# Optimization experiments

Hardware: AMD Instinct MI355X
Metric: run time of the kernel (lower is better)

Reference implementation:

```python
import jax, jax.numpy as jnp
import numpy as np
from math import sqrt

D_LLM = 768
N_HEADS = 8
D_KEYS = 128


def setup_inputs() -> dict:
    key = jax.random.key(0)
    ks = jax.random.split(key, 9)
    B, T, N, S = 8, 96, 16, 1000
    dkh = D_KEYS * N_HEADS
    inp = {
        "time_series": jax.random.normal(ks[0], (B, T, N), dtype=jnp.float32),
        "source_embedding": jax.random.normal(ks[1], (S, D_LLM), dtype=jnp.float32),
        "value_embedding": jax.random.normal(ks[2], (S, D_LLM), dtype=jnp.float32),
        # key_projection: Linear(d_llm, d_keys*n_heads)
        "Wk": jax.random.normal(ks[3], (D_LLM, dkh), dtype=jnp.float32) / np.float32(sqrt(D_LLM)),
        "bk": jnp.zeros((dkh,), dtype=jnp.float32),
        # value_projection: Linear(d_llm, d_keys*n_heads)
        "Wv": jax.random.normal(ks[4], (D_LLM, dkh), dtype=jnp.float32) / np.float32(sqrt(D_LLM)),
        "bv": jnp.zeros((dkh,), dtype=jnp.float32),
        # out_projection: Linear(d_keys*n_heads, d_llm)
        "Wo": jax.random.normal(ks[5], (dkh, D_LLM), dtype=jnp.float32) / np.float32(sqrt(dkh)),
        "bo": jnp.zeros((D_LLM,), dtype=jnp.float32),
    }
    return inp


def reference(time_series, source_embedding, value_embedding, Wk, bk, Wv, bv, Wo, bo):
    B, T, N = time_series.shape
    S = source_embedding.shape[0]
    H, dk = N_HEADS, D_KEYS

    # (B,T,N) -> (B*N, T); Q repeats each scalar across d_keys*n_heads then nan->0
    ts = jnp.transpose(time_series, (0, 2, 1)).reshape(B * N, T)
    ts = jnp.where(jnp.isnan(ts), jnp.float32(0.0), ts)
    Q = jnp.broadcast_to(ts[:, :, None, None], (B * N, T, H, dk))  # bthe

    K = (source_embedding @ Wk + bk).reshape(S, H, dk)  # she
    V = (value_embedding @ Wv + bv).reshape(S, H, dk)   # she

    scale = jnp.float32(1.0 / sqrt(dk))
    scores = jnp.einsum('bthe,she->bhts', Q, K)          # [B*N, H, T, S]
    A = jax.nn.softmax(scale * scores, axis=-1)          # dropout = identity (eval)
    out = jnp.einsum('bhts,she->bthe', A, V).reshape(B * N, T, H * dk)
    return out @ Wo + bo                                 # [B*N, T, d_llm]
```

## Files before the change

kernel.cpp:

```cpp
#include <hip/hip_runtime.h>
#include <hip/hip_bf16.h>
#include <math.h>

#define D_LLM 768
#define DKH   1024
#define NH    8
#define DK    128
#define S_LEN 1000
#define S_PAD 1024
#define M_ROWS 12288
#define T_LEN 96
#define N_VARS 16

static constexpr float SCALE_EXP2 = (float)(0.08838834764831845 * 1.4426950408889634);

typedef __attribute__((ext_vector_type(8))) _Float16 half8;
typedef __attribute__((ext_vector_type(2))) _Float16 half2v;
typedef __attribute__((ext_vector_type(4))) float f32x4;

__device__ __forceinline__ half2v pkrtz(float a, float b) {
    return __builtin_bit_cast(half2v, __builtin_amdgcn_cvt_pkrtz(a, b));
}

__device__ __forceinline__ void gload_lds16(const void* g, void* l) {
    __builtin_amdgcn_global_load_lds(
        (const __attribute__((address_space(1))) unsigned int*)g,
        (__attribute__((address_space(3))) unsigned int*)l, 16, 0, 0);
}

__global__ __launch_bounds__(256) void prep_kernel(const float* __restrict__ vemb,
                                                   const float* __restrict__ Wv,
                                                   const float* __restrict__ Wo,
                                                   const float* __restrict__ Wk,
                                                   const float* __restrict__ bk,
                                                   _Float16* __restrict__ Ab16,
                                                   _Float16* __restrict__ Wvt,
                                                   _Float16* __restrict__ Wot,
                                                   float* __restrict__ Wksum,
                                                   float* __restrict__ bksum) {
    __shared__ float tl[32][33];
    int blk = blockIdx.x, tid = threadIdx.x;
    if (blk < 768) {
        int i4 = (blk * 256 + tid) * 4;
        float4 v = make_float4(0.f, 0.f, 0.f, 0.f);
        if (i4 < S_LEN * D_LLM) v = *(const float4*)(vemb + i4);
        short4 o;
        o.x = __builtin_bit_cast(short, (_Float16)v.x);
        o.y = __builtin_bit_cast(short, (_Float16)v.y);
        o.z = __builtin_bit_cast(short, (_Float16)v.z);
        o.w = __builtin_bit_cast(short, (_Float16)v.w);
        *(short4*)(Ab16 + i4) = o;
    } else if (blk < 1536) {
        int tau = blk - 768;
        int k0 = (tau % 24) * 32, n0 = (tau / 24) * 32;
        int tx = tid & 31, ty = tid >> 5;
        #pragma unroll
        for (int p = 0; p < 4; ++p)
            tl[ty + p * 8][tx] = Wv[(size_t)(k0 + ty + p * 8) * DKH + n0 + tx];
        __syncthreads();
        #pragma unroll
        for (int p = 0; p < 4; ++p)
            Wvt[(size_t)(n0 + ty + p * 8) * D_LLM + k0 + tx] = (_Float16)tl[tx][ty + p * 8];
    } else if (blk < 2304) {
        int tau = blk - 1536;
        int k0 = (tau & 31) * 32, n0 = (tau >> 5) * 32;
        int tx = tid & 31, ty = tid >> 5;
        #pragma unroll
        for (int p = 0; p < 4; ++p)
            tl[ty + p * 8][tx] = Wo[(size_t)(k0 + ty + p * 8) * D_LLM + n0 + tx];
        __syncthreads();
        #pragma unroll
        for (int p = 0; p < 4; ++p)
            Wot[(size_t)(n0 + ty + p * 8) * DKH + k0 + tx] = (_Float16)tl[tx][ty + p * 8];
    } else {
        int blk2 = blk - 2304;
        int w = tid >> 6, lane = tid & 63;
        if (blk2 < 192) {
            int d = blk2 * 4 + w;
            const float* p = Wk + (size_t)d * DKH + lane * 16;
            float s = 0.f;
            #pragma unroll
            for (int i = 0; i < 4; ++i) {
                float4 v = *(const float4*)(p + i * 4);
                s += v.x + v.y + v.z + v.w;
            }
            s += __shfl_down(s, 4);
            s += __shfl_down(s, 2);
            s += __shfl_down(s, 1);
            if ((lane & 7) == 0) Wksum[d * NH + (lane >> 3)] = s;
        } else if (w == 0) {
            const float* p = bk + lane * 16;
            float s = 0.f;
            #pragma unroll
            for (int i = 0; i < 4; ++i) {
                float4 v = *(const float4*)(p + i * 4);
                s += v.x + v.y + v.z + v.w;
            }
            s += __shfl_down(s, 4);
            s += __shfl_down(s, 2);
            s += __shfl_down(s, 1);
            if ((lane & 7) == 0) bksum[lane >> 3] = s;
        }
    }
}

__global__ __launch_bounds__(256) void ksum_kernel(const float* __restrict__ src,
                                                   const float* __restrict__ Wksum,
                                                   const float* __restrict__ bksum,
                                                   float* __restrict__ Kpad) {
    int w = threadIdx.x >> 6, lane = threadIdx.x & 63;
    int s = blockIdx.x * 4 + w;
    if (s >= S_LEN) {
        if (lane < 8) Kpad[lane * S_PAD + s] = 0.f;
        return;
    }
    const float* sp = src + (size_t)s * D_LLM + lane * 12;
    float xv[12];
    ((float4*)xv)[0] = *(const float4*)(sp);
    ((float4*)xv)[1] = *(const float4*)(sp + 4);
    ((float4*)xv)[2] = *(const float4*)(sp + 8);
    float a[8] = {0.f, 0.f, 0.f, 0.f, 0.f, 0.f, 0.f, 0.f};
    const float* wp = Wksum + lane * 12 * NH;
    #pragma unroll
    for (int i = 0; i < 12; ++i) {
        float4 wa = *(const float4*)(wp + i * 8);
        float4 wb = *(const float4*)(wp + i * 8 + 4);
        a[0] = fmaf(xv[i], wa.x, a[0]); a[1] = fmaf(xv[i], wa.y, a[1]);
        a[2] = fmaf(xv[i], wa.z, a[2]); a[3] = fmaf(xv[i], wa.w, a[3]);
        a[4] = fmaf(xv[i], wb.x, a[4]); a[5] = fmaf(xv[i], wb.y, a[5]);
        a[6] = fmaf(xv[i], wb.z, a[6]); a[7] = fmaf(xv[i], wb.w, a[7]);
    }
    #pragma unroll
    for (int off = 32; off > 0; off >>= 1) {
        #pragma unroll
        for (int hh = 0; hh < 8; ++hh) a[hh] += __shfl_xor(a[hh], off);
    }
    #pragma unroll
    for (int hh = 0; hh < 8; ++hh)
        if (lane == hh) Kpad[hh * S_PAD + s] = (a[hh] + bksum[hh]) * SCALE_EXP2;
}

__global__ __launch_bounds__(64) void kminmax_kernel(const float* __restrict__ Kpad,
                                                     float* __restrict__ mnmx) {
    int h = blockIdx.x, lane = threadIdx.x;
    float mx = -1e30f, mn = 1e30f;
    for (int s = lane; s < S_LEN; s += 64) {
        float v = Kpad[h * S_PAD + s];
        mx = fmaxf(mx, v); mn = fminf(mn, v);
    }
    #pragma unroll
    for (int off = 32; off > 0; off >>= 1) {
        mx = fmaxf(mx, __shfl_xor(mx, off));
        mn = fminf(mn, __shfl_xor(mn, off));
    }
    if (lane == 0) { mnmx[h * 2] = mn; mnmx[h * 2 + 1] = mx; }
}

__global__ __launch_bounds__(256) void vproj_kernel(const _Float16* __restrict__ A,
                                                    const _Float16* __restrict__ Bt,
                                                    const float* __restrict__ bias,
                                                    _Float16* __restrict__ Vt) {
    __shared__ _Float16 As[2][64 * 32];
    __shared__ _Float16 Bs[2][64 * 32];
    int t = threadIdx.x, w = t >> 6, lane = t & 63;
    int bm0 = (blockIdx.x >> 4) * 64, bn0 = (blockIdx.x & 15) * 64;
    int lrow = t >> 2, lcol = (t & 3) * 8;
    const _Float16* ga = A + (size_t)(bm0 + lrow) * D_LLM + lcol;
    const _Float16* gb = Bt + (size_t)(bn0 + lrow) * D_LLM + lcol;

    f32x4 acc[2][2];
    #pragma unroll
    for (int m = 0; m < 2; ++m)
        #pragma unroll
        for (int n = 0; n < 2; ++n) acc[m][n] = (f32x4){0.f, 0.f, 0.f, 0.f};
    int sgrp = (lane >> 4) << 3;
    int arow = (w >> 1) * 32 + (lane & 15);
    int brow = (w & 1) * 32 + (lane & 15);

#define VSTAGE(buf, k0) do { \
        gload_lds16(ga + (k0), (char*)&As[buf][0] + w * 1024); \
        gload_lds16(gb + (k0), (char*)&Bs[buf][0] + w * 1024); } while (0)

    VSTAGE(0, 0);
    __syncthreads();
    #pragma unroll 2
    for (int tt = 0; tt < 24; ++tt) {
        int cur = tt & 1;
        if (tt < 23) VSTAGE(cur ^ 1, (tt + 1) * 32);
        const _Float16* Ac = &As[cur][0];
        const _Float16* Bc = &Bs[cur][0];
        half8 af[2], bf[2];
        #pragma unroll
        for (int m = 0; m < 2; ++m) af[m] = *(const half8*)(Ac + (arow + m * 16) * 32 + sgrp);
        #pragma unroll
        for (int n = 0; n < 2; ++n) bf[n] = *(const half8*)(Bc + (brow + n * 16) * 32 + sgrp);
        __builtin_amdgcn_s_setprio(1);
        #pragma unroll
        for (int m = 0; m < 2; ++m)
            #pragma unroll
            for (int n = 0; n < 2; ++n)
                acc[m][n] = __builtin_amdgcn_mfma_f32_16x16x32_f16(af[m], bf[n], acc[m][n], 0, 0, 0);
        __builtin_amdgcn_s_setprio(0);
        __syncthreads();
    }
#undef VSTAGE

    int rowoff = (lane >> 4) << 2;
    #pragma unroll
    for (int m = 0; m < 2; ++m) {
        #pragma unroll
        for (int n = 0; n < 2; ++n) {
            int c = bn0 + (w & 1) * 32 + n * 16 + (lane & 15);
            float b = bias[c];
            #pragma unroll
            for (int q = 0; q < 4; ++q) {
                int srow = bm0 + (w >> 1) * 32 + m * 16 + rowoff + q;
                float val = (srow < S_LEN) ? acc[m][n][q] + b : 0.f;
                Vt[(size_t)c * S_PAD + srow] = (_Float16)val;
            }
        }
    }
}

__device__ __forceinline__ void compute_afr(const float* kq, float x0, float x1,
                                            float nm0, float nm1, half8& o0, half8& o1) {
    float4 a = *(const float4*)kq;
    float4 b = *(const float4*)(kq + 4);
    float kv[8] = {a.x, a.y, a.z, a.w, b.x, b.y, b.z, b.w};
    union { half8 v; half2v h[4]; } u0, u1;
    #pragma unroll
    for (int j = 0; j < 4; ++j) {
        float w00 = __builtin_amdgcn_exp2f(fmaf(x0, kv[2 * j], nm0));
        float w01 = __builtin_amdgcn_exp2f(fmaf(x0, kv[2 * j + 1], nm0));
        u0.h[j] = pkrtz(w00, w01);
        float w10 = __builtin_amdgcn_exp2f(fmaf(x1, kv[2 * j], nm1));
        float w11 = __builtin_amdgcn_exp2f(fmaf(x1, kv[2 * j + 1], nm1));
        u1.h[j] = pkrtz(w10, w11);
    }
    o0 = u0.v; o1 = u1.v;
}

__global__ __launch_bounds__(256) void attn_mfma_kernel(const float* __restrict__ ts,
                                                        const float* __restrict__ Kpad,
                                                        const float* __restrict__ mnmx,
                                                        const _Float16* __restrict__ Vt,
                                                        _Float16* __restrict__ attB) {
    __shared__ _Float16 Vs[2][8192];
    const int tid = threadIdx.x;
    const int lane = tid & 63, w = tid >> 6;
    const int h = blockIdx.y;
    const int m0 = (blockIdx.x * 4 + w) * 32;
    const int l15 = lane & 15, q = lane >> 4;

    const int erow = w * 8 + (lane >> 3);
    const int sgl = ((lane & 7) ^ (lane >> 3)) * 8;
    const _Float16* gsrc = Vt + (size_t)(h * DK + erow) * S_PAD + sgl;

    float mn = mnmx[h * 2], mx = mnmx[h * 2 + 1];
    float x0, x1, nm0, nm1;
    {
        int m = m0 + l15;
        int rr = m / T_LEN;
        float v = ts[((size_t)(rr >> 4) * T_LEN + (m % T_LEN)) * N_VARS + (rr & 15)];
        x0 = (v != v) ? 0.f : v;
        nm0 = -((x0 >= 0.f) ? x0 * mx : x0 * mn);
        m = m0 + 16 + l15;
        rr = m / T_LEN;
        v = ts[((size_t)(rr >> 4) * T_LEN + (m % T_LEN)) * N_VARS + (rr & 15)];
        x1 = (v != v) ? 0.f : v;
        nm1 = -((x1 >= 0.f) ? x1 * mx : x1 * mn);
    }
    float wpadf0, wpadf1;
    {
        half2v p0 = pkrtz(__builtin_amdgcn_exp2f(nm0), 0.f);
        half2v p1 = pkrtz(__builtin_amdgcn_exp2f(nm1), 0.f);
        wpadf0 = (float)p0[0];
        wpadf1 = (float)p1[0];
    }

    f32x4 acc0[8], acc1[8];
    #pragma unroll
    for (int e = 0; e < 8; ++e) {
        acc0[e] = (f32x4){0.f, 0.f, 0.f, 0.f};
        acc1[e] = (f32x4){0.f, 0.f, 0.f, 0.f};
    }
    f32x4 accd0 = (f32x4){0.f, 0.f, 0.f, 0.f};
    f32x4 accd1 = (f32x4){0.f, 0.f, 0.f, 0.f};
    half8 ones;
    #pragma unroll
    for (int j = 0; j < 8; ++j) ones[j] = (_Float16)1.0f;

    const float* kvp = Kpad + h * S_PAD + q * 8;
    half8 afrA0, afrA1, afrB0, afrB1;
    compute_afr(kvp, x0, x1, nm0, nm1, afrA0, afrA1);

    #pragma unroll
    for (int i = 0; i < 4; ++i)
        gload_lds16(gsrc + (size_t)(i * 32) * S_PAD, (char*)&Vs[0][0] + i * 4096 + w * 1024);
    #pragma unroll
    for (int i = 0; i < 4; ++i)
        gload_lds16(gsrc + (size_t)(i * 32) * S_PAD + 64, (char*)&Vs[1][0] + i * 4096 + w * 1024);
    asm volatile("s_waitcnt vmcnt(4)" ::: "memory");
    __builtin_amdgcn_s_barrier();

    const int bofs0 = l15 * 128 + ((q * 16) ^ ((l15 & 7) << 4));
    const int bofs1 = l15 * 128 + ((64 + q * 16) ^ ((l15 & 7) << 4));

#define PVSTEP(AF0, AF1, BOFS) do { \
        __builtin_amdgcn_s_setprio(1); \
        _Pragma("unroll") \
        for (int e = 0; e < 8; ++e) { \
            half8 bfv = *(const half8*)(cb + e * 2048 + (BOFS)); \
            acc0[e] = __builtin_amdgcn_mfma_f32_16x16x32_f16(AF0, bfv, acc0[e], 0, 0, 0); \
            acc1[e] = __builtin_amdgcn_mfma_f32_16x16x32_f16(AF1, bfv, acc1[e], 0, 0, 0); \
        } \
        accd0 = __builtin_amdgcn_mfma_f32_16x16x32_f16(AF0, ones, accd0, 0, 0, 0); \
        accd1 = __builtin_amdgcn_mfma_f32_16x16x32_f16(AF1, ones, accd1, 0, 0, 0); \
        __builtin_amdgcn_s_setprio(0); } while (0)

    #pragma unroll 2
    for (int kt = 0; kt < 16; ++kt) {
        const char* cb = (const char*)&Vs[0][0] + (kt & 1) * 16384;
        compute_afr(kvp + kt * 64 + 32, x0, x1, nm0, nm1, afrB0, afrB1);
        PVSTEP(afrA0, afrA1, bofs0);
        if (kt < 15) compute_afr(kvp + (kt + 1) * 64, x0, x1, nm0, nm1, afrA0, afrA1);
        PVSTEP(afrB0, afrB1, bofs1);
        __builtin_amdgcn_s_barrier();
        if (kt < 14) {
            #pragma unroll
            for (int i = 0; i < 4; ++i)
                gload_lds16(gsrc + (size_t)(i * 32) * S_PAD + (kt + 2) * 64,
                            (char*)&Vs[0][0] + (kt & 1) * 16384 + i * 4096 + w * 1024);
            asm volatile("s_waitcnt vmcnt(4)" ::: "memory");
        } else {
            asm volatile("s_waitcnt vmcnt(0)" ::: "memory");
        }
        __builtin_amdgcn_s_barrier();
    }
#undef PVSTEP

    int rowoff = q << 2;
    #pragma unroll
    for (int r = 0; r < 2; ++r) {
        #pragma unroll
        for (int qq = 0; qq < 4; ++qq) {
            float wp = __shfl(r ? wpadf1 : wpadf0, rowoff + qq);
            float den = (r ? accd1[qq] : accd0[qq]) - 24.f * wp;
            float inv = 1.f / den;
            int mrow = m0 + r * 16 + rowoff + qq;
            _Float16* op = attB + (size_t)mrow * DKH + h * DK + l15;
            #pragma unroll
            for (int e = 0; e < 8; ++e)
                op[e * 16] = (_Float16)((r ? acc1[e][qq] : acc0[e][qq]) * inv);
        }
    }
}

__global__ __launch_bounds__(256) void outproj_kernel(const _Float16* __restrict__ A,
                                                      const _Float16* __restrict__ Bt,
                                                      const float* __restrict__ bo,
                                                      float* __restrict__ C) {
    __shared__ _Float16 As[2][128 * 32];
    __shared__ _Float16 Bs[2][96 * 32];
    int wg = blockIdx.x;
    wg = (wg & 7) * 96 + (wg >> 3);
    int bx = wg & 7, by = wg >> 3;
    int t = threadIdx.x, w = t >> 6, lane = t & 63;
    int bm0 = by * 128, bn0 = bx * 96;
    int lrow = t >> 2, lcol = (t & 3) * 8;
    const _Float16* ga0 = A + (size_t)(bm0 + lrow) * DKH + lcol;
    const _Float16* ga1 = ga0 + (size_t)64 * DKH;
    const _Float16* gb0 = Bt + (size_t)(bn0 + lrow) * DKH + lcol;
    const _Float16* gb1 = gb0 + (size_t)64 * DKH;

    f32x4 acc[4][3];
    #pragma unroll
    for (int m = 0; m < 4; ++m)
        #pragma unroll
        for (int n = 0; n < 3; ++n) acc[m][n] = (f32x4){0.f, 0.f, 0.f, 0.f};

    int sgrp = (lane >> 4) << 3;
    int arow = (w >> 1) * 64 + (lane & 15);
    int brow = (w & 1) * 48 + (lane & 15);

#define OSTAGE(buf, k0) do { \
        gload_lds16(ga0 + (k0), (char*)&As[buf][0] + w * 1024); \
        gload_lds16(ga1 + (k0), (char*)&As[buf][0] + 4096 + w * 1024); \
        gload_lds16(gb0 + (k0), (char*)&Bs[buf][0] + w * 1024); \
        if (w < 2) gload_lds16(gb1 + (k0), (char*)&Bs[buf][0] + 4096 + w * 1024); } while (0)

    OSTAGE(0, 0);
    __syncthreads();
    #pragma unroll 2
    for (int tt = 0; tt < 32; ++tt) {
        int cur = tt & 1;
        if (tt < 31) OSTAGE(cur ^ 1, (tt + 1) * 32);
        const _Float16* Ac = &As[cur][0];
        const _Float16* Bc = &Bs[cur][0];
        half8 af[4], bf[3];
        #pragma unroll
        for (int m = 0; m < 4; ++m) af[m] = *(const half8*)(Ac + (arow + m * 16) * 32 + sgrp);
        #pragma unroll
        for (int n = 0; n < 3; ++n) bf[n] = *(const half8*)(Bc + (brow + n * 16) * 32 + sgrp);
        __builtin_amdgcn_s_setprio(1);
        #pragma unroll
        for (int m = 0; m < 4; ++m)
            #pragma unroll
            for (int n = 0; n < 3; ++n)
                acc[m][n] = __builtin_amdgcn_mfma_f32_16x16x32_f16(af[m], bf[n], acc[m][n], 0, 0, 0);
        __builtin_amdgcn_s_setprio(0);
        __syncthreads();
    }
#undef OSTAGE

    int rowoff = (lane >> 4) << 2;
    #pragma unroll
    for (int m = 0; m < 4; ++m) {
        #pragma unroll
        for (int n = 0; n < 3; ++n) {
            int col = bn0 + (w & 1) * 48 + n * 16 + (lane & 15);
            float b = bo[col];
            #pragma unroll
            for (int q = 0; q < 4; ++q) {
                int row = bm0 + (w >> 1) * 64 + m * 16 + rowoff + q;
                C[(size_t)row * D_LLM + col] = acc[m][n][q] + b;
            }
        }
    }
}

extern "C" void kernel_launch(void* const* d_in, const int* in_sizes, int n_in,
                              void* d_out, int out_size, void* d_ws, size_t ws_size,
                              hipStream_t stream) {
    const float* ts   = (const float*)d_in[0];
    const float* src  = (const float*)d_in[1];
    const float* vemb = (const float*)d_in[2];
    const float* Wk   = (const float*)d_in[3];
    const float* bk   = (const float*)d_in[4];
    const float* Wv   = (const float*)d_in[5];
    const float* bv   = (const float*)d_in[6];
    const float* Wo   = (const float*)d_in[7];
    const float* bo   = (const float*)d_in[8];
    float* out = (float*)d_out;

    float* ws = (float*)d_ws;
    float* Kpad   = ws;
    float* Wksum  = ws + 8192;
    float* bksum  = ws + 14336;
    float* mnmx   = ws + 14352;
    _Float16* Vt   = (_Float16*)(ws + 14592);
    _Float16* Wot  = (_Float16*)(ws + 540672);
    _Float16* attB = (_Float16*)(ws + 936960);
    _Float16* Ab16 = (_Float16*)(ws + 936960);
    _Float16* Wvt  = (_Float16*)(ws + 1330176);

    prep_kernel<<<2497, 256, 0, stream>>>(vemb, Wv, Wo, Wk, bk, Ab16, Wvt, Wot, Wksum, bksum);
    ksum_kernel<<<256, 256, 0, stream>>>(src, Wksum, bksum, Kpad);
    kminmax_kernel<<<8, 64, 0, stream>>>(Kpad, mnmx);
    vproj_kernel<<<256, 256, 0, stream>>>(Ab16, Wvt, bv, Vt);
    {
        dim3 g(96, NH);
        attn_mfma_kernel<<<g, 256, 0, stream>>>(ts, Kpad, mnmx, Vt, attB);
    }
    outproj_kernel<<<768, 256, 0, stream>>>(attB, Wot, bo, out);
}
```

Baseline: 100.8 us.

## Merge K-sum and V-projection kernels, fold min/max into attention, triple-buffer loads

Merges the K row-sum kernel and the V projection GEMM into one launch split by block index, and drops the separate min/max kernel. Each attention block now loads its K row into LDS and computes the per-head min/max itself. The attention and output-projection loops move from double to triple-buffered LDS staging with one barrier per iteration and explicit vmcnt waits, so global loads overlap compute more. This removes two launches and some barriers, at the cost of more LDS per block (possible occupancy loss) and redundant min/max work in every attention block.

```diff
diff --git a/kernel.cpp b/kernel.cpp
--- a/kernel.cpp
+++ b/kernel.cpp
@@ -104,67 +104,54 @@
     }
 }
 
-__global__ __launch_bounds__(256) void ksum_kernel(const float* __restrict__ src,
-                                                   const float* __restrict__ Wksum,
-                                                   const float* __restrict__ bksum,
-                                                   float* __restrict__ Kpad) {
-    int w = threadIdx.x >> 6, lane = threadIdx.x & 63;
-    int s = blockIdx.x * 4 + w;
-    if (s >= S_LEN) {
-        if (lane < 8) Kpad[lane * S_PAD + s] = 0.f;
+__global__ __launch_bounds__(256) void kv_kernel(const float* __restrict__ src,
+                                                 const float* __restrict__ Wksum,
+                                                 const float* __restrict__ bksum,
+                                                 float* __restrict__ Kpad,
+                                                 const _Float16* __restrict__ A,
+                                                 const _Float16* __restrict__ Bt,
+                                                 const float* __restrict__ bias,
+                                                 _Float16* __restrict__ Vt) {
+    __shared__ _Float16 VAs[2][2048];
+    __shared__ _Float16 VBs[2][2048];
+    int tid = threadIdx.x;
+    if (blockIdx.x < 256) {
+        int w = tid >> 6, lane = tid & 63;
+        int s = blockIdx.x * 4 + w;
+        if (s >= S_LEN) {
+            if (lane < 8) Kpad[lane * S_PAD + s] = 0.f;
+            return;
+        }
+        const float* sp = src + (size_t)s * D_LLM + lane * 12;
+        float xv[12];
+        ((float4*)xv)[0] = *(const float4*)(sp);
+        ((float4*)xv)[1] = *(const float4*)(sp + 4);
+        ((float4*)xv)[2] = *(const float4*)(sp + 8);
+        float a[8] = {0.f, 0.f, 0.f, 0.f, 0.f, 0.f, 0.f, 0.f};
+        const float* wp = Wksum + lane * 12 * NH;
+        #pragma unroll
+        for (int i = 0; i < 12; ++i) {
+            float4 wa = *(const float4*)(wp + i * 8);
+            float4 wb = *(const float4*)(wp + i * 8 + 4);
+            a[0] = fmaf(xv[i], wa.x, a[0]); a[1] = fmaf(xv[i], wa.y, a[1]);
+            a[2] = fmaf(xv[i], wa.z, a[2]); a[3] = fmaf(xv[i], wa.w, a[3]);
+            a[4] = fmaf(xv[i], wb.x, a[4]); a[5] = fmaf(xv[i], wb.y, a[5]);
+            a[6] = fmaf(xv[i], wb.z, a[6]); a[7] = fmaf(xv[i], wb.w, a[7]);
+        }
+        #pragma unroll
+        for (int off = 32; off > 0; off >>= 1) {
+            #pragma unroll
+            for (int hh = 0; hh < 8; ++hh) a[hh] += __shfl_xor(a[hh], off);
+        }
+        #pragma unroll
+        for (int hh = 0; hh < 8; ++hh)
+            if (lane == hh) Kpad[hh * S_PAD + s] = (a[hh] + bksum[hh]) * SCALE_EXP2;
         return;
     }
-    const float* sp = src + (size_t)s * D_LLM + lane * 12;
-    float xv[12];
-    ((float4*)xv)[0] = *(const float4*)(sp);
-    ((float4*)xv)[1] = *(const float4*)(sp + 4);
-    ((float4*)xv)[2] = *(const float4*)(sp + 8);
-    float a[8] = {0.f, 0.f, 0.f, 0.f, 0.f, 0.f, 0.f, 0.f};
-    const float* wp = Wksum + lane * 12 * NH;
-    #pragma unroll
-    for (int i = 0; i < 12; ++i) {
-        float4 wa = *(const float4*)(wp + i * 8);
-        float4 wb = *(const float4*)(wp + i * 8 + 4);
-        a[0] = fmaf(xv[i], wa.x, a[0]); a[1] = fmaf(xv[i], wa.y, a[1]);
-        a[2] = fmaf(xv[i], wa.z, a[2]); a[3] = fmaf(xv[i], wa.w, a[3]);
-        a[4] = fmaf(xv[i], wb.x, a[4]); a[5] = fmaf(xv[i], wb.y, a[5]);
-        a[6] = fmaf(xv[i], wb.z, a[6]); a[7] = fmaf(xv[i], wb.w, a[7]);
-    }
-    #pragma unroll
-    for (int off = 32; off > 0; off >>= 1) {
-        #pragma unroll
-        for (int hh = 0; hh < 8; ++hh) a[hh] += __shfl_xor(a[hh], off);
-    }
-    #pragma unroll
-    for (int hh = 0; hh < 8; ++hh)
-        if (lane == hh) Kpad[hh * S_PAD + s] = (a[hh] + bksum[hh]) * SCALE_EXP2;
-}
-
-__global__ __launch_bounds__(64) void kminmax_kernel(const float* __restrict__ Kpad,
-                                                     float* __restrict__ mnmx) {
-    int h = blockIdx.x, lane = threadIdx.x;
-    float mx = -1e30f, mn = 1e30f;
-    for (int s = lane; s < S_LEN; s += 64) {
-        float v = Kpad[h * S_PAD + s];
-        mx = fmaxf(mx, v); mn = fminf(mn, v);
-    }
-    #pragma unroll
-    for (int off = 32; off > 0; off >>= 1) {
-        mx = fmaxf(mx, __shfl_xor(mx, off));
-        mn = fminf(mn, __shfl_xor(mn, off));
-    }
-    if (lane == 0) { mnmx[h * 2] = mn; mnmx[h * 2 + 1] = mx; }
-}
-
-__global__ __launch_bounds__(256) void vproj_kernel(const _Float16* __restrict__ A,
-                                                    const _Float16* __restrict__ Bt,
-                                                    const float* __restrict__ bias,
-                                                    _Float16* __restrict__ Vt) {
-    __shared__ _Float16 As[2][64 * 32];
-    __shared__ _Float16 Bs[2][64 * 32];
-    int t = threadIdx.x, w = t >> 6, lane = t & 63;
-    int bm0 = (blockIdx.x >> 4) * 64, bn0 = (blockIdx.x & 15) * 64;
-    int lrow = t >> 2, lcol = (t & 3) * 8;
+    int b2 = blockIdx.x - 256;
+    int w = tid >> 6, lane = tid & 63;
+    int bm0 = (b2 >> 4) * 64, bn0 = (b2 & 15) * 64;
+    int lrow = tid >> 2, lcol = (tid & 3) * 8;
     const _Float16* ga = A + (size_t)(bm0 + lrow) * D_LLM + lcol;
     const _Float16* gb = Bt + (size_t)(bn0 + lrow) * D_LLM + lcol;
 
@@ -178,8 +165,8 @@
     int brow = (w & 1) * 32 + (lane & 15);
 
 #define VSTAGE(buf, k0) do { \
-        gload_lds16(ga + (k0), (char*)&As[buf][0] + w * 1024); \
-        gload_lds16(gb + (k0), (char*)&Bs[buf][0] + w * 1024); } while (0)
+        gload_lds16(ga + (k0), (char*)&VAs[buf][0] + w * 1024); \
+        gload_lds16(gb + (k0), (char*)&VBs[buf][0] + w * 1024); } while (0)
 
     VSTAGE(0, 0);
     __syncthreads();
@@ -187,8 +174,8 @@
     for (int tt = 0; tt < 24; ++tt) {
         int cur = tt & 1;
         if (tt < 23) VSTAGE(cur ^ 1, (tt + 1) * 32);
-        const _Float16* Ac = &As[cur][0];
-        const _Float16* Bc = &Bs[cur][0];
+        const _Float16* Ac = &VAs[cur][0];
+        const _Float16* Bc = &VBs[cur][0];
         half8 af[2], bf[2];
         #pragma unroll
         for (int m = 0; m < 2; ++m) af[m] = *(const half8*)(Ac + (arow + m * 16) * 32 + sgrp);
@@ -242,10 +229,11 @@
 
 __global__ __launch_bounds__(256) void attn_mfma_kernel(const float* __restrict__ ts,
                                                         const float* __restrict__ Kpad,
-                                                        const float* __restrict__ mnmx,
                                                         const _Float16* __restrict__ Vt,
                                                         _Float16* __restrict__ attB) {
-    __shared__ _Float16 Vs[2][8192];
+    __shared__ _Float16 Vs[3][8192];
+    __shared__ float Krow[1024];
+    __shared__ float red[8];
     const int tid = threadIdx.x;
     const int lane = tid & 63, w = tid >> 6;
     const int h = blockIdx.y;
@@ -255,21 +243,54 @@
     const int erow = w * 8 + (lane >> 3);
     const int sgl = ((lane & 7) ^ (lane >> 3)) * 8;
     const _Float16* gsrc = Vt + (size_t)(h * DK + erow) * S_PAD + sgl;
-
-    float mn = mnmx[h * 2], mx = mnmx[h * 2 + 1];
-    float x0, x1, nm0, nm1;
+    const float* kg = Kpad + h * S_PAD;
+
+    gload_lds16(kg + w * 256 + lane * 4, (char*)Krow + w * 1024);
+    #pragma unroll
+    for (int i = 0; i < 4; ++i)
+        gload_lds16(gsrc + (size_t)(i * 32) * S_PAD, (char*)&Vs[0][0] + i * 4096 + w * 1024);
+    #pragma unroll
+    for (int i = 0; i < 4; ++i)
+        gload_lds16(gsrc + (size_t)(i * 32) * S_PAD + 64, (char*)&Vs[1][0] + i * 4096 + w * 1024);
+
+    float x0, x1;
     {
         int m = m0 + l15;
         int rr = m / T_LEN;
         float v = ts[((size_t)(rr >> 4) * T_LEN + (m % T_LEN)) * N_VARS + (rr & 15)];
         x0 = (v != v) ? 0.f : v;
-        nm0 = -((x0 >= 0.f) ? x0 * mx : x0 * mn);
         m = m0 + 16 + l15;
         rr = m / T_LEN;
         v = ts[((size_t)(rr >> 4) * T_LEN + (m % T_LEN)) * N_VARS + (rr & 15)];
         x1 = (v != v) ? 0.f : v;
-        nm1 = -((x1 >= 0.f) ? x1 * mx : x1 * mn);
-    }
+    }
+
+    asm volatile("s_waitcnt vmcnt(8)" ::: "memory");
+    __builtin_amdgcn_sched_barrier(0);
+    __builtin_amdgcn_s_barrier();
+
+    float mn, mx;
+    {
+        float4 k4 = *(const float4*)&Krow[tid * 4];
+        if (tid < 250) {
+            mx = fmaxf(fmaxf(k4.x, k4.y), fmaxf(k4.z, k4.w));
+            mn = fminf(fminf(k4.x, k4.y), fminf(k4.z, k4.w));
+        } else { mx = -3e38f; mn = 3e38f; }
+        #pragma unroll
+        for (int off = 32; off > 0; off >>= 1) {
+            mx = fmaxf(mx, __shfl_xor(mx, off));
+            mn = fminf(mn, __shfl_xor(mn, off));
+        }
+        if (lane == 0) { red[w * 2] = mn; red[w * 2 + 1] = mx; }
+        asm volatile("s_waitcnt lgkmcnt(0)" ::: "memory");
+        __builtin_amdgcn_sched_barrier(0);
+        __builtin_amdgcn_s_barrier();
+        mn = fminf(fminf(red[0], red[2]), fminf(red[4], red[6]));
+        mx = fmaxf(fmaxf(red[1], red[3]), fmaxf(red[5], red[7]));
+    }
+
+    float nm0 = -((x0 >= 0.f) ? x0 * mx : x0 * mn);
+    float nm1 = -((x1 >= 0.f) ? x1 * mx : x1 * mn);
     float wpadf0, wpadf1;
     {
         half2v p0 = pkrtz(__builtin_amdgcn_exp2f(nm0), 0.f);
@@ -290,18 +311,9 @@
     #pragma unroll
     for (int j = 0; j < 8; ++j) ones[j] = (_Float16)1.0f;
 
-    const float* kvp = Kpad + h * S_PAD + q * 8;
+    const float* kvp = Krow + q * 8;
     half8 afrA0, afrA1, afrB0, afrB1;
     compute_afr(kvp, x0, x1, nm0, nm1, afrA0, afrA1);
-
-    #pragma unroll
-    for (int i = 0; i < 4; ++i)
-        gload_lds16(gsrc + (size_t)(i * 32) * S_PAD, (char*)&Vs[0][0] + i * 4096 + w * 1024);
-    #pragma unroll
-    for (int i = 0; i < 4; ++i)
-        gload_lds16(gsrc + (size_t)(i * 32) * S_PAD + 64, (char*)&Vs[1][0] + i * 4096 + w * 1024);
-    asm volatile("s_waitcnt vmcnt(4)" ::: "memory");
-    __builtin_amdgcn_s_barrier();
 
     const int bofs0 = l15 * 128 + ((q * 16) ^ ((l15 & 7) << 4));
     const int bofs1 = l15 * 128 + ((64 + q * 16) ^ ((l15 & 7) << 4));
@@ -318,24 +330,23 @@
         accd1 = __builtin_amdgcn_mfma_f32_16x16x32_f16(AF1, ones, accd1, 0, 0, 0); \
         __builtin_amdgcn_s_setprio(0); } while (0)
 
-    #pragma unroll 2
+    #pragma unroll
     for (int kt = 0; kt < 16; ++kt) {
-        const char* cb = (const char*)&Vs[0][0] + (kt & 1) * 16384;
+        if (kt == 15) asm volatile("s_waitcnt vmcnt(0)" ::: "memory");
+        else         asm volatile("s_waitcnt vmcnt(4)" ::: "memory");
+        __builtin_amdgcn_sched_barrier(0);
+        __builtin_amdgcn_s_barrier();
+        if (kt < 14) {
+            char* d = (char*)&Vs[0][0] + ((kt + 2) % 3) * 16384 + w * 1024;
+            #pragma unroll
+            for (int i = 0; i < 4; ++i)
+                gload_lds16(gsrc + (size_t)(i * 32) * S_PAD + (kt + 2) * 64, d + i * 4096);
+        }
+        const char* cb = (const char*)&Vs[0][0] + (kt % 3) * 16384;
         compute_afr(kvp + kt * 64 + 32, x0, x1, nm0, nm1, afrB0, afrB1);
         PVSTEP(afrA0, afrA1, bofs0);
         if (kt < 15) compute_afr(kvp + (kt + 1) * 64, x0, x1, nm0, nm1, afrA0, afrA1);
         PVSTEP(afrB0, afrB1, bofs1);
-        __builtin_amdgcn_s_barrier();
-        if (kt < 14) {
-            #pragma unroll
-            for (int i = 0; i < 4; ++i)
-                gload_lds16(gsrc + (size_t)(i * 32) * S_PAD + (kt + 2) * 64,
-                            (char*)&Vs[0][0] + (kt & 1) * 16384 + i * 4096 + w * 1024);
-            asm volatile("s_waitcnt vmcnt(4)" ::: "memory");
-        } else {
-            asm volatile("s_waitcnt vmcnt(0)" ::: "memory");
-        }
-        __builtin_amdgcn_s_barrier();
     }
 #undef PVSTEP
 
@@ -360,8 +371,8 @@
                                                       const _Float16* __restrict__ Bt,
                                                       const float* __restrict__ bo,
                                                       float* __restrict__ C) {
-    __shared__ _Float16 As[2][128 * 32];
-    __shared__ _Float16 Bs[2][96 * 32];
+    __shared__ _Float16 As[3][4096];
+    __shared__ _Float16 Bs[3][3072];
     int wg = blockIdx.x;
     wg = (wg & 7) * 96 + (wg >> 3);
     int bx = wg & 7, by = wg >> 3;
@@ -383,20 +394,24 @@
     int arow = (w >> 1) * 64 + (lane & 15);
     int brow = (w & 1) * 48 + (lane & 15);
 
-#define OSTAGE(buf, k0) do { \
-        gload_lds16(ga0 + (k0), (char*)&As[buf][0] + w * 1024); \
-        gload_lds16(ga1 + (k0), (char*)&As[buf][0] + 4096 + w * 1024); \
-        gload_lds16(gb0 + (k0), (char*)&Bs[buf][0] + w * 1024); \
-        if (w < 2) gload_lds16(gb1 + (k0), (char*)&Bs[buf][0] + 4096 + w * 1024); } while (0)
+#define OSTAGE(bi, k0) do { \
+        gload_lds16(ga0 + (k0), (char*)&As[bi][0] + w * 1024); \
+        gload_lds16(ga1 + (k0), (char*)&As[bi][0] + 4096 + w * 1024); \
+        gload_lds16(gb0 + (k0), (char*)&Bs[bi][0] + w * 1024); \
+        if (w < 2) gload_lds16(gb1 + (k0), (char*)&Bs[bi][0] + 4096 + w * 1024); } while (0)
 
     OSTAGE(0, 0);
-    __syncthreads();
-    #pragma unroll 2
-    for (int tt = 0; tt < 32; ++tt) {
-        int cur = tt & 1;
-        if (tt < 31) OSTAGE(cur ^ 1, (tt + 1) * 32);
-        const _Float16* Ac = &As[cur][0];
-        const _Float16* Bc = &Bs[cur][0];
+    OSTAGE(1, 32);
+    #pragma unroll
+    for (int kt = 0; kt < 32; ++kt) {
+        if (kt == 31)   asm volatile("s_waitcnt vmcnt(0)" ::: "memory");
+        else if (w < 2) asm volatile("s_waitcnt vmcnt(4)" ::: "memory");
+        else            asm volatile("s_waitcnt vmcnt(3)" ::: "memory");
+        __builtin_amdgcn_sched_barrier(0);
+        __builtin_amdgcn_s_barrier();
+        if (kt < 30) OSTAGE((kt + 2) % 3, (kt + 2) * 32);
+        const _Float16* Ac = &As[kt % 3][0];
+        const _Float16* Bc = &Bs[kt % 3][0];
         half8 af[4], bf[3];
         #pragma unroll
         for (int m = 0; m < 4; ++m) af[m] = *(const half8*)(Ac + (arow + m * 16) * 32 + sgrp);
@@ -409,7 +424,6 @@
             for (int n = 0; n < 3; ++n)
                 acc[m][n] = __builtin_amdgcn_mfma_f32_16x16x32_f16(af[m], bf[n], acc[m][n], 0, 0, 0);
         __builtin_amdgcn_s_setprio(0);
-        __syncthreads();
     }
 #undef OSTAGE
 
@@ -447,7 +461,6 @@
     float* Kpad   = ws;
     float* Wksum  = ws + 8192;
     float* bksum  = ws + 14336;
-    float* mnmx   = ws + 14352;
     _Float16* Vt   = (_Float16*)(ws + 14592);
     _Float16* Wot  = (_Float16*)(ws + 540672);
     _Float16* attB = (_Float16*)(ws + 936960);
@@ -455,12 +468,10 @@
     _Float16* Wvt  = (_Float16*)(ws + 1330176);
 
     prep_kernel<<<2497, 256, 0, stream>>>(vemb, Wv, Wo, Wk, bk, Ab16, Wvt, Wot, Wksum, bksum);
-    ksum_kernel<<<256, 256, 0, stream>>>(src, Wksum, bksum, Kpad);
-    kminmax_kernel<<<8, 64, 0, stream>>>(Kpad, mnmx);
-    vproj_kernel<<<256, 256, 0, stream>>>(Ab16, Wvt, bv, Vt);
+    kv_kernel<<<512, 256, 0, stream>>>(src, Wksum, bksum, Kpad, Ab16, Wvt, bv, Vt);
     {
         dim3 g(96, NH);
-        attn_mfma_kernel<<<g, 256, 0, stream>>>(ts, Kpad, mnmx, Vt, attB);
+        attn_mfma_kernel<<<g, 256, 0, stream>>>(ts, Kpad, Vt, attB);
     }
     outproj_kernel<<<768, 256, 0, stream>>>(attB, Wot, bo, out);
 }
```

Measured after the change: 87.95 us (median of 2 runs). -12.8%, faster.
